# Kernel optimization log

Hardware: AMD Instinct MI355X
Metric: run time of the kernel (lower is better)

## Reference

```python
import jax, jax.numpy as jnp
import numpy as np

DIM = 4096
N_Q_HEADS = 32
N_KV_HEADS = 8
HEAD_DIM = DIM // N_Q_HEADS  # 128
N_REPS = N_Q_HEADS // N_KV_HEADS  # 4
MAX_SEQ = 4096
BATCH = 8
SEQ = 1
START_POS = MAX_SEQ - SEQ  # 4095 (decode step)


def setup_inputs() -> dict:
    key = jax.random.key(0)
    ks = jax.random.split(key, 8)
    s = 0.02
    x = jax.random.normal(ks[0], (BATCH, SEQ, DIM), dtype=jnp.float32)
    wq = jax.random.normal(ks[1], (DIM, N_Q_HEADS * HEAD_DIM), dtype=jnp.float32) * s
    wk = jax.random.normal(ks[2], (DIM, N_KV_HEADS * HEAD_DIM), dtype=jnp.float32) * s
    wv = jax.random.normal(ks[3], (DIM, N_KV_HEADS * HEAD_DIM), dtype=jnp.float32) * s
    wo = jax.random.normal(ks[4], (N_Q_HEADS * HEAD_DIM, DIM), dtype=jnp.float32) * s
    # pre-populated KV cache (decode scenario)
    cache_keys = jax.random.normal(ks[5], (BATCH, MAX_SEQ, N_KV_HEADS, HEAD_DIM), dtype=jnp.float32)
    cache_values = jax.random.normal(ks[6], (BATCH, MAX_SEQ, N_KV_HEADS, HEAD_DIM), dtype=jnp.float32)
    # true RoPE frequencies for positions [START_POS, START_POS+SEQ)
    inv_freq = 1.0 / (10000.0 ** (np.arange(0, HEAD_DIM, 2, dtype=np.float32) / HEAD_DIM))
    pos = np.arange(START_POS, START_POS + SEQ, dtype=np.float32)
    angles = pos[:, None] * inv_freq[None, :]  # [SEQ, HEAD_DIM//2]
    freqs_cos = jnp.asarray(np.cos(angles), dtype=jnp.float32)
    freqs_sin = jnp.asarray(np.sin(angles), dtype=jnp.float32)
    return dict(x=x, start_pos=STAR_POS_INT(), freqs_cos=freqs_cos, freqs_sin=freqs_sin,
                wq=wq, wk=wk, wv=wv, wo=wo,
                cache_keys=cache_keys, cache_values=cache_values)


def STAR_POS_INT():
    return STAR_POS if False else START_POS


def _apply_rope(x, cos, sin):
    # x: [B, S, H, hd]; cos/sin: [S, hd//2]
    xr = x[..., 0::2]
    xi = x[..., 1::2]
    c = cos[None, :, None, :]
    s = sin[None, :, None, :]
    out_r = xr * c - xi * s
    out_i = xr * s + xi * c
    # interleave back: [..., hd//2, 2] -> [..., hd]
    out = jnp.stack([out_r, out_i], axis=-1)
    return out.reshape(x.shape)


def reference(x, start_pos, freqs_cos, freqs_sin, wq, wk, wv, wo, cache_keys, cache_values):
    B, S, _ = x.shape
    q = (x @ wq).reshape(B, S, N_Q_HEADS, HEAD_DIM)
    k = (x @ wk).reshape(B, S, N_KV_HEADS, HEAD_DIM)
    v = (x @ wv).reshape(B, S, N_KV_HEADS, HEAD_DIM)
    q = _apply_rope(q, freqs_cos, freqs_sin)
    k = _apply_rope(k, freqs_cos, freqs_sin)
    # KV-cache scatter write (static start_pos)
    cache_keys = cache_keys.at[:B, start_pos:start_pos + S].set(jax.lax.stop_gradient(k))
    cache_values = cache_values.at[:B, start_pos:start_pos + S].set(jax.lax.stop_gradient(v))
    total = start_pos + S
    keys = cache_keys[:B, :total]     # [B, T, Hkv, hd]
    values = cache_values[:B, :total]
    # repeat_kv: [B, T, Hkv, hd] -> [B, T, Hq, hd]
    keys = jnp.repeat(keys, N_REPS, axis=2)
    values = jnp.repeat(values, N_REPS, axis=2)
    # attention
    scale = 1.0 / jnp.sqrt(jnp.float32(HEAD_DIM))
    scores = jnp.einsum('bshd,bthd->bhst', q, keys) * scale  # [B, Hq, S, T]
    mask = (jnp.arange(total)[None, :] <= (jnp.arange(S)[:, None] + start_pos))  # [S, T]
    scores = jnp.where(mask[None, None], scores, -1e9)
    attn = jax.nn.softmax(scores, axis=-1)
    out = jnp.einsum('bhst,bthd->bshd', attn, values)  # [B, S, Hq, hd]
    out = out.reshape(B, S, N_Q_HEADS * HEAD_DIM)
    return out @ wo
```

## Files before the change

### kernel.cpp

```cpp
#include <hip/hip_runtime.h>

#define DIM 4096
#define HD 128
#define NQH 32
#define NKVH 8
#define NB 8
#define MAXSEQ 4096
#define TOTALT 4096
#define QCOLS (NQH*HD)
#define KVCOLS (NKVH*HD)
#define CCOLS (QCOLS + 2*KVCOLS)
#define DCH 64
#define KSP (DIM/DCH)
#define SUB 32
#define NSUB 16
#define CHK (SUB*NSUB)
#define NCHB (TOTALT/CHK)

typedef __attribute__((address_space(1))) const void __gvoid;
typedef __attribute__((address_space(3))) void __lvoid;
#define GLD16(g, l) __builtin_amdgcn_global_load_lds((__gvoid*)(g), (__lvoid*)(l), 16, 0, 0)
#define VMWAIT(N) asm volatile("s_waitcnt vmcnt(" #N ")" ::: "memory")
#define LGKMWAIT0 asm volatile("s_waitcnt lgkmcnt(0)" ::: "memory")
#define SCHEDBAR __builtin_amdgcn_sched_barrier(0)

__global__ __launch_bounds__(128) void gemv4_kernel(
    const float* __restrict__ x, const float* __restrict__ wq,
    const float* __restrict__ wk, const float* __restrict__ wv,
    float* __restrict__ part, int pstride)
{
    __shared__ float xs[DCH*NB];
    const int tx = threadIdx.x;
    const int d0 = blockIdx.y*DCH;
    for (int i = tx; i < DCH*NB; i += 128)
        xs[(i&63)*NB + (i>>6)] = x[(i>>6)*DIM + d0 + (i&63)];
    __syncthreads();

    const int colbase = blockIdx.x*512;
    const float* w; int wcols, wcol;
    if (colbase < QCOLS)               { w = wq; wcols = QCOLS;  wcol = colbase; }
    else if (colbase < QCOLS+KVCOLS)   { w = wk; wcols = KVCOLS; wcol = colbase - QCOLS; }
    else                               { w = wv; wcols = KVCOLS; wcol = colbase - QCOLS - KVCOLS; }

    const float* wp = w + (size_t)d0*wcols + wcol + tx*4;
    float4 a[NB];
    #pragma unroll
    for (int b = 0; b < NB; b++) { a[b].x=0.f; a[b].y=0.f; a[b].z=0.f; a[b].w=0.f; }

    #pragma unroll 4
    for (int dl = 0; dl < DCH; dl++) {
        float4 wv4 = *reinterpret_cast<const float4*>(wp + (size_t)dl*wcols);
        float4 x0 = *reinterpret_cast<const float4*>(&xs[dl*NB]);
        float4 x1 = *reinterpret_cast<const float4*>(&xs[dl*NB + 4]);
        a[0].x += wv4.x*x0.x; a[0].y += wv4.y*x0.x; a[0].z += wv4.z*x0.x; a[0].w += wv4.w*x0.x;
        a[1].x += wv4.x*x0.y; a[1].y += wv4.y*x0.y; a[1].z += wv4.z*x0.y; a[1].w += wv4.w*x0.y;
        a[2].x += wv4.x*x0.z; a[2].y += wv4.y*x0.z; a[2].z += wv4.z*x0.z; a[2].w += wv4.w*x0.z;
        a[3].x += wv4.x*x0.w; a[3].y += wv4.y*x0.w; a[3].z += wv4.z*x0.w; a[3].w += wv4.w*x0.w;
        a[4].x += wv4.x*x1.x; a[4].y += wv4.y*x1.x; a[4].z += wv4.z*x1.x; a[4].w += wv4.w*x1.x;
        a[5].x += wv4.x*x1.y; a[5].y += wv4.y*x1.y; a[5].z += wv4.z*x1.y; a[5].w += wv4.w*x1.y;
        a[6].x += wv4.x*x1.z; a[6].y += wv4.y*x1.z; a[6].z += wv4.z*x1.z; a[6].w += wv4.w*x1.z;
        a[7].x += wv4.x*x1.w; a[7].y += wv4.y*x1.w; a[7].z += wv4.z*x1.w; a[7].w += wv4.w*x1.w;
    }
    const int ocol = colbase + tx*4;
    #pragma unroll
    for (int b = 0; b < NB; b++)
        *reinterpret_cast<float4*>(&part[((size_t)(blockIdx.y*NB + b))*pstride + ocol]) = a[b];
}

__global__ __launch_bounds__(256) void qkv_reduce_rope(
    const float* __restrict__ part, const float* __restrict__ fc,
    const float* __restrict__ fs, float* __restrict__ q,
    float* __restrict__ knew, float* __restrict__ vnew)
{
    const int p = blockIdx.x*256 + threadIdx.x;
    const int b = p / (CCOLS/2);
    const int c0 = (p % (CCOLS/2))*2;
    float s0 = 0.f, s1 = 0.f;
    const float* pb = part + (size_t)b*CCOLS + c0;
    #pragma unroll 8
    for (int ky = 0; ky < KSP; ky++) {
        float2 v = *reinterpret_cast<const float2*>(pb + (size_t)ky*NB*CCOLS);
        s0 += v.x; s1 += v.y;
    }
    float r0 = s0, r1 = s1;
    if (c0 < QCOLS + KVCOLS) {
        int i = (c0 & (HD-1)) >> 1;
        float c = fc[i], s = fs[i];
        r0 = s0*c - s1*s;
        r1 = s0*s + s1*c;
    }
    if (c0 < QCOLS) {
        *reinterpret_cast<float2*>(&q[b*QCOLS + c0]) = make_float2(r0, r1);
    } else if (c0 < QCOLS + KVCOLS) {
        *reinterpret_cast<float2*>(&knew[b*KVCOLS + (c0 - QCOLS)]) = make_float2(r0, r1);
    } else {
        *reinterpret_cast<float2*>(&vnew[b*KVCOLS + (c0 - QCOLS - KVCOLS)]) = make_float2(r0, r1);
    }
}

__global__ __launch_bounds__(256) void attn_stream_kernel(
    const float* __restrict__ q, const float* __restrict__ knew,
    const float* __restrict__ vnew, const float* __restrict__ K,
    const float* __restrict__ V, float* __restrict__ pout,
    float* __restrict__ pml)
{
    __shared__ float ks[2][SUB*HD];
    __shared__ float vs_[2][SUB*HD];
    __shared__ __align__(16) float psf[SUB*4];
    __shared__ float ps2[16*HD];

    const int tx = threadIdx.x;
    const int chunk = blockIdx.x, kvh = blockIdx.y, b = blockIdx.z;
    const size_t blkid = (size_t)(b*NKVH + kvh)*NCHB + chunk;
    const int lane = tx & 63, j = tx >> 6;
    const int r = lane & 31, h = lane >> 5;
    const size_t kvstride = (size_t)NKVH*HD;
    const size_t kbase0 = ((size_t)(b*MAXSEQ + chunk*CHK)*NKVH + kvh)*HD;
    const bool lastChunk = (chunk == NCHB-1);
    const int wseg = (tx & 192)*4;

    auto stage = [&](int nb, int srow, bool lastT) {
        #pragma unroll
        for (int k = 0; k < 4; k++) {
            int F = k*256 + tx;
            int t = F >> 5, sw = F & 31;
            int i = sw ^ t;
            const float* srck = (lastT && t == SUB-1)
                ? (knew + (b*NKVH + kvh)*HD + i*4)
                : (K + kbase0 + (size_t)(srow + t)*kvstride + i*4);
            GLD16(srck, &ks[nb][k*1024 + wseg]);
            const float* srcv = (lastT && t == SUB-1)
                ? (vnew + (b*NKVH + kvh)*HD + sw*4)
                : (V + kbase0 + (size_t)(srow + t)*kvstride + sw*4);
            GLD16(srcv, &vs_[nb][k*1024 + wseg]);
        }
    };

    float4 qreg[16];
    {
        const float4* qg = reinterpret_cast<const float4*>(
            q + b*QCOLS + (kvh*4 + j)*HD + h*64);
        #pragma unroll
        for (int c = 0; c < 16; c++) qreg[c] = qg[c];
    }
    stage(0, 0, false);

    float2 acc[4];
    #pragma unroll
    for (int hh = 0; hh < 4; hh++) acc[hh] = make_float2(0.f, 0.f);
    float l_lane = 0.f;

    for (int s = 0; s < NSUB; ++s) {
        const int cb = s & 1;
        if (s+1 < NSUB) {
            stage(cb^1, (s+1)*SUB, lastChunk && (s+1 == NSUB-1));
            VMWAIT(8);
        } else {
            VMWAIT(0);
        }
        __builtin_amdgcn_s_barrier();
        SCHEDBAR;

        float sj = 0.f;
        {
            const float* kc = ks[cb];
            #pragma unroll
            for (int c = 0; c < 16; c++) {
                int i = h*16 + c;
                float4 kv = *reinterpret_cast<const float4*>(&kc[(r*32 + (i ^ r))*4]);
                float4 qv = qreg[c];
                sj += kv.x*qv.x + kv.y*qv.y + kv.z*qv.z + kv.w*qv.w;
            }
        }
        sj += __shfl_xor(sj, 32, 64);
        sj *= 0.08838834764831845f;
        float p = __expf(sj);
        l_lane += p;
        if (h == 0) psf[r*4 + j] = p;
        LGKMWAIT0; SCHEDBAR;
        __builtin_amdgcn_s_barrier();
        SCHEDBAR;

        {
            const float* vc = vs_[cb];
            #pragma unroll
            for (int t = 0; t < 8; t++) {
                int row = j*8 + t;
                float4 pg = *reinterpret_cast<const float4*>(&psf[row*4]);
                float2 vv = *reinterpret_cast<const float2*>(&vc[row*HD + lane*2]);
                acc[0].x += pg.x*vv.x; acc[0].y += pg.x*vv.y;
                acc[1].x += pg.y*vv.x; acc[1].y += pg.y*vv.y;
                acc[2].x += pg.z*vv.x; acc[2].y += pg.z*vv.y;
                acc[3].x += pg.w*vv.x; acc[3].y += pg.w*vv.y;
            }
        }
        LGKMWAIT0; SCHEDBAR;
        __builtin_amdgcn_s_barrier();
        SCHEDBAR;
    }

    #pragma unroll
    for (int hh = 0; hh < 4; hh++)
        *reinterpret_cast<float2*>(&ps2[(j*4 + hh)*HD + lane*2]) = acc[hh];
    #pragma unroll
    for (int k = 16; k >= 1; k >>= 1) l_lane += __shfl_xor(l_lane, k, 64);
    if (lane == 0) pml[blkid*4 + j] = l_lane;
    __syncthreads();
    {
        const int hh = tx >> 6;
        const int d0 = (tx & 63)*2;
        float sx = 0.f, sy = 0.f;
        #pragma unroll
        for (int w = 0; w < 4; w++) {
            float2 v = *reinterpret_cast<const float2*>(&ps2[(w*4 + hh)*HD + d0]);
            sx += v.x; sy += v.y;
        }
        *reinterpret_cast<float2*>(pout + blkid*512 + hh*HD + d0) = make_float2(sx, sy);
    }
}

__global__ __launch_bounds__(128) void attn_combine_kernel(
    const float* __restrict__ pout, const float* __restrict__ pml,
    float* __restrict__ attn_out)
{
    const int d = threadIdx.x;
    const int qh = blockIdx.x;
    const int b = blockIdx.y;
    const int kvh = qh >> 2, j = qh & 3;
    const size_t base = (size_t)(b*NKVH + kvh)*NCHB;
    float L = 0.f, acc = 0.f;
    #pragma unroll
    for (int i = 0; i < NCHB; i++) {
        L   += pml[(base + i)*4 + j];
        acc += pout[(base + i)*512 + j*HD + d];
    }
    attn_out[b*QCOLS + qh*HD + d] = acc / L;
}

__global__ __launch_bounds__(256) void wo_reduce_kernel(
    const float* __restrict__ part, float* __restrict__ out)
{
    const int g = blockIdx.x*256 + threadIdx.x;
    float sx = 0.f, sy = 0.f;
    #pragma unroll 8
    for (int ky = 0; ky < KSP; ky++) {
        float2 v = *reinterpret_cast<const float2*>(part + (size_t)ky*NB*QCOLS + g*2);
        sx += v.x; sy += v.y;
    }
    *reinterpret_cast<float2*>(out + g*2) = make_float2(sx, sy);
}

extern "C" void kernel_launch(void* const* d_in, const int* in_sizes, int n_in,
                              void* d_out, int out_size, void* d_ws, size_t ws_size,
                              hipStream_t stream)
{
    const float* x  = (const float*)d_in[0];
    const float* fc = (const float*)d_in[2];
    const float* fs = (const float*)d_in[3];
    const float* wq = (const float*)d_in[4];
    const float* wk = (const float*)d_in[5];
    const float* wv = (const float*)d_in[6];
    const float* wo = (const float*)d_in[7];
    const float* K  = (const float*)d_in[8];
    const float* V  = (const float*)d_in[9];

    float* ws     = (float*)d_ws;
    float* q      = ws;
    float* knew   = ws + 32768;
    float* vnew   = ws + 40960;
    float* attn_o = ws + 49152;
    float* qkvp   = ws + 81920;
    float* pout   = ws + 3227648;
    float* pml    = ws + 3489792;
    float* wop    = ws + 81920;

    gemv4_kernel<<<dim3(CCOLS/512, KSP), dim3(128), 0, stream>>>(x, wq, wk, wv, qkvp, CCOLS);
    qkv_reduce_rope<<<dim3(NB*CCOLS/2/256), dim3(256), 0, stream>>>(qkvp, fc, fs, q, knew, vnew);
    attn_stream_kernel<<<dim3(NCHB, NKVH, NB), dim3(256), 0, stream>>>(q, knew, vnew, K, V, pout, pml);
    attn_combine_kernel<<<dim3(NQH, NB), dim3(128), 0, stream>>>(pout, pml, attn_o);
    gemv4_kernel<<<dim3(QCOLS/512, KSP), dim3(128), 0, stream>>>(attn_o, wo, wo, wo, wop, QCOLS);
    wo_reduce_kernel<<<dim3(NB*QCOLS/2/256), dim3(256), 0, stream>>>(wop, (float*)d_out);
}
```

Baseline: 119.9 us.

## Process all KV heads per block over contiguous full cache rows

The attention streaming kernel now gives each block a 128-timestep chunk covering all 8 KV heads, staging full contiguous 4KB cache rows, 8 rows per tile, instead of strided per-head 512B segments. It uses 512 threads, one wave per KV head, with an XOR swizzle to avoid LDS bank conflicts. The goal is more sequential DRAM access for the dominant KV-cache read. In exchange the grid halves to 256 blocks and each block takes about 128KB of double-buffered LDS, which limits a CU to one resident block. The per-chunk partial outputs also grow, so the combine kernel has more data to write and read.

```diff
diff --git a/kernel.cpp b/kernel.cpp
--- a/kernel.cpp
+++ b/kernel.cpp
@@ -12,10 +12,10 @@
 #define CCOLS (QCOLS + 2*KVCOLS)
 #define DCH 64
 #define KSP (DIM/DCH)
-#define SUB 32
-#define NSUB 16
-#define CHK (SUB*NSUB)
-#define NCHB (TOTALT/CHK)
+#define RT 8
+#define NT 16
+#define CHKR (RT*NT)
+#define NCHK (TOTALT/CHKR)
 
 typedef __attribute__((address_space(1))) const void __gvoid;
 typedef __attribute__((address_space(3))) void __lvoid;
@@ -98,62 +98,64 @@
     }
 }
 
-__global__ __launch_bounds__(256) void attn_stream_kernel(
+__global__ __launch_bounds__(512) void attn_fullrow_kernel(
     const float* __restrict__ q, const float* __restrict__ knew,
     const float* __restrict__ vnew, const float* __restrict__ K,
     const float* __restrict__ V, float* __restrict__ pout,
     float* __restrict__ pml)
 {
-    __shared__ float ks[2][SUB*HD];
-    __shared__ float vs_[2][SUB*HD];
-    __shared__ __align__(16) float psf[SUB*4];
-    __shared__ float ps2[16*HD];
+    __shared__ float ks[2][RT*KVCOLS];
+    __shared__ float vs[2][RT*KVCOLS];
+    __shared__ __align__(16) float psf[NKVH*RT*4];
 
     const int tx = threadIdx.x;
-    const int chunk = blockIdx.x, kvh = blockIdx.y, b = blockIdx.z;
-    const size_t blkid = (size_t)(b*NKVH + kvh)*NCHB + chunk;
-    const int lane = tx & 63, j = tx >> 6;
-    const int r = lane & 31, h = lane >> 5;
-    const size_t kvstride = (size_t)NKVH*HD;
-    const size_t kbase0 = ((size_t)(b*MAXSEQ + chunk*CHK)*NKVH + kvh)*HD;
-    const bool lastChunk = (chunk == NCHB-1);
-    const int wseg = (tx & 192)*4;
+    const int chunk = blockIdx.x, b = blockIdx.y;
+    const int w = tx >> 6, lane = tx & 63;
+    const int r = lane >> 3, seg = lane & 7;
+    const size_t blkid = (size_t)b*NCHK + chunk;
+    const size_t base0 = ((size_t)b*MAXSEQ + (size_t)chunk*CHKR)*KVCOLS;
+    const bool lastChunk = (chunk == NCHK-1);
 
     auto stage = [&](int nb, int srow, bool lastT) {
         #pragma unroll
         for (int k = 0; k < 4; k++) {
-            int F = k*256 + tx;
-            int t = F >> 5, sw = F & 31;
-            int i = sw ^ t;
-            const float* srck = (lastT && t == SUB-1)
-                ? (knew + (b*NKVH + kvh)*HD + i*4)
-                : (K + kbase0 + (size_t)(srow + t)*kvstride + i*4);
-            GLD16(srck, &ks[nb][k*1024 + wseg]);
-            const float* srcv = (lastT && t == SUB-1)
-                ? (vnew + (b*NKVH + kvh)*HD + sw*4)
-                : (V + kbase0 + (size_t)(srow + t)*kvstride + sw*4);
-            GLD16(srcv, &vs_[nb][k*1024 + wseg]);
+            const int Lbase = k*512 + w*64;
+            const int rr = Lbase >> 8;
+            const int L = Lbase + lane;
+            const int g = L & 255;
+            const int gk = (g & ~7) | ((g & 7) ^ rr);
+            const float* srck = (lastT && rr == RT-1)
+                ? (knew + b*KVCOLS + gk*4)
+                : (K + base0 + (size_t)(srow + rr)*KVCOLS + gk*4);
+            GLD16(srck, &ks[nb][(size_t)Lbase*4]);
+            const float* srcv = (lastT && rr == RT-1)
+                ? (vnew + b*KVCOLS + g*4)
+                : (V + base0 + (size_t)(srow + rr)*KVCOLS + g*4);
+            GLD16(srcv, &vs[nb][(size_t)Lbase*4]);
         }
     };
 
     float4 qreg[16];
     {
-        const float4* qg = reinterpret_cast<const float4*>(
-            q + b*QCOLS + (kvh*4 + j)*HD + h*64);
-        #pragma unroll
-        for (int c = 0; c < 16; c++) qreg[c] = qg[c];
+        #pragma unroll
+        for (int hh = 0; hh < 4; hh++) {
+            const float4* qg = reinterpret_cast<const float4*>(
+                q + b*QCOLS + (w*4 + hh)*HD + seg*16);
+            #pragma unroll
+            for (int c = 0; c < 4; c++) qreg[hh*4 + c] = qg[c];
+        }
     }
     stage(0, 0, false);
 
     float2 acc[4];
     #pragma unroll
     for (int hh = 0; hh < 4; hh++) acc[hh] = make_float2(0.f, 0.f);
-    float l_lane = 0.f;
-
-    for (int s = 0; s < NSUB; ++s) {
+    float l_acc[4] = {0.f, 0.f, 0.f, 0.f};
+
+    for (int s = 0; s < NT; ++s) {
         const int cb = s & 1;
-        if (s+1 < NSUB) {
-            stage(cb^1, (s+1)*SUB, lastChunk && (s+1 == NSUB-1));
+        if (s+1 < NT) {
+            stage(cb^1, (s+1)*RT, lastChunk && (s+1 == NT-1));
             VMWAIT(8);
         } else {
             VMWAIT(0);
@@ -161,33 +163,44 @@
         __builtin_amdgcn_s_barrier();
         SCHEDBAR;
 
-        float sj = 0.f;
+        float s4[4] = {0.f, 0.f, 0.f, 0.f};
         {
             const float* kc = ks[cb];
             #pragma unroll
-            for (int c = 0; c < 16; c++) {
-                int i = h*16 + c;
-                float4 kv = *reinterpret_cast<const float4*>(&kc[(r*32 + (i ^ r))*4]);
-                float4 qv = qreg[c];
-                sj += kv.x*qv.x + kv.y*qv.y + kv.z*qv.z + kv.w*qv.w;
+            for (int c = 0; c < 4; c++) {
+                int g  = w*32 + seg*4 + c;
+                int gs = (g & ~7) | ((g & 7) ^ r);
+                float4 kv = *reinterpret_cast<const float4*>(&kc[(r*256 + gs)*4]);
+                #pragma unroll
+                for (int hh = 0; hh < 4; hh++) {
+                    float4 qv = qreg[hh*4 + c];
+                    s4[hh] += kv.x*qv.x + kv.y*qv.y + kv.z*qv.z + kv.w*qv.w;
+                }
             }
         }
-        sj += __shfl_xor(sj, 32, 64);
-        sj *= 0.08838834764831845f;
-        float p = __expf(sj);
-        l_lane += p;
-        if (h == 0) psf[r*4 + j] = p;
+        #pragma unroll
+        for (int m = 1; m <= 4; m <<= 1) {
+            #pragma unroll
+            for (int hh = 0; hh < 4; hh++) s4[hh] += __shfl_xor(s4[hh], m, 64);
+        }
+        float p0 = __expf(s4[0]*0.08838834764831845f);
+        float p1 = __expf(s4[1]*0.08838834764831845f);
+        float p2 = __expf(s4[2]*0.08838834764831845f);
+        float p3 = __expf(s4[3]*0.08838834764831845f);
+        l_acc[0] += p0; l_acc[1] += p1; l_acc[2] += p2; l_acc[3] += p3;
+        if (seg == 0)
+            *reinterpret_cast<float4*>(&psf[(w*RT + r)*4]) = make_float4(p0, p1, p2, p3);
         LGKMWAIT0; SCHEDBAR;
         __builtin_amdgcn_s_barrier();
         SCHEDBAR;
 
         {
-            const float* vc = vs_[cb];
-            #pragma unroll
-            for (int t = 0; t < 8; t++) {
-                int row = j*8 + t;
-                float4 pg = *reinterpret_cast<const float4*>(&psf[row*4]);
-                float2 vv = *reinterpret_cast<const float2*>(&vc[row*HD + lane*2]);
+            const float* vc = vs[cb];
+            #pragma unroll
+            for (int t = 0; t < RT; t++) {
+                float4 pg = *reinterpret_cast<const float4*>(&psf[(w*RT + t)*4]);
+                float2 vv = *reinterpret_cast<const float2*>(
+                    &vc[t*KVCOLS + w*HD + lane*2]);
                 acc[0].x += pg.x*vv.x; acc[0].y += pg.x*vv.y;
                 acc[1].x += pg.y*vv.x; acc[1].y += pg.y*vv.y;
                 acc[2].x += pg.z*vv.x; acc[2].y += pg.z*vv.y;
@@ -201,21 +214,17 @@
 
     #pragma unroll
     for (int hh = 0; hh < 4; hh++)
-        *reinterpret_cast<float2*>(&ps2[(j*4 + hh)*HD + lane*2]) = acc[hh];
-    #pragma unroll
-    for (int k = 16; k >= 1; k >>= 1) l_lane += __shfl_xor(l_lane, k, 64);
-    if (lane == 0) pml[blkid*4 + j] = l_lane;
-    __syncthreads();
-    {
-        const int hh = tx >> 6;
-        const int d0 = (tx & 63)*2;
-        float sx = 0.f, sy = 0.f;
-        #pragma unroll
-        for (int w = 0; w < 4; w++) {
-            float2 v = *reinterpret_cast<const float2*>(&ps2[(w*4 + hh)*HD + d0]);
-            sx += v.x; sy += v.y;
-        }
-        *reinterpret_cast<float2*>(pout + blkid*512 + hh*HD + d0) = make_float2(sx, sy);
+        *reinterpret_cast<float2*>(
+            pout + blkid*4096 + (w*4 + hh)*HD + lane*2) = acc[hh];
+    #pragma unroll
+    for (int m = 1; m <= 32; m <<= 1) {
+        #pragma unroll
+        for (int hh = 0; hh < 4; hh++) l_acc[hh] += __shfl_xor(l_acc[hh], m, 64);
+    }
+    if (lane == 0) {
+        #pragma unroll
+        for (int hh = 0; hh < 4; hh++)
+            pml[blkid*NQH + w*4 + hh] = l_acc[hh]*0.125f;
     }
 }
 
@@ -226,13 +235,12 @@
     const int d = threadIdx.x;
     const int qh = blockIdx.x;
     const int b = blockIdx.y;
-    const int kvh = qh >> 2, j = qh & 3;
-    const size_t base = (size_t)(b*NKVH + kvh)*NCHB;
     float L = 0.f, acc = 0.f;
-    #pragma unroll
-    for (int i = 0; i < NCHB; i++) {
-        L   += pml[(base + i)*4 + j];
-        acc += pout[(base + i)*512 + j*HD + d];
+    #pragma unroll 8
+    for (int i = 0; i < NCHK; i++) {
+        const size_t blkid = (size_t)b*NCHK + i;
+        L   += pml[blkid*NQH + qh];
+        acc += pout[blkid*4096 + qh*HD + d];
     }
     attn_out[b*QCOLS + qh*HD + d] = acc / L;
 }
@@ -271,12 +279,12 @@
     float* attn_o = ws + 49152;
     float* qkvp   = ws + 81920;
     float* pout   = ws + 3227648;
-    float* pml    = ws + 3489792;
+    float* pml    = ws + 4276224;
     float* wop    = ws + 81920;
 
     gemv4_kernel<<<dim3(CCOLS/512, KSP), dim3(128), 0, stream>>>(x, wq, wk, wv, qkvp, CCOLS);
     qkv_reduce_rope<<<dim3(NB*CCOLS/2/256), dim3(256), 0, stream>>>(qkvp, fc, fs, q, knew, vnew);
-    attn_stream_kernel<<<dim3(NCHB, NKVH, NB), dim3(256), 0, stream>>>(q, knew, vnew, K, V, pout, pml);
+    attn_fullrow_kernel<<<dim3(NCHK, NB), dim3(512), 0, stream>>>(q, knew, vnew, K, V, pout, pml);
     attn_combine_kernel<<<dim3(NQH, NB), dim3(128), 0, stream>>>(pout, pml, attn_o);
     gemv4_kernel<<<dim3(QCOLS/512, KSP), dim3(128), 0, stream>>>(attn_o, wo, wo, wo, wop, QCOLS);
     wo_reduce_kernel<<<dim3(NB*QCOLS/2/256), dim3(256), 0, stream>>>(wop, (float*)d_out);
```

New measurement: 128.7 us. 7.3% more time.

## Stream V directly from global memory and shrink attention chunks for more blocks

Applied to the files above, without the earlier changes.

The attention kernel now stages only K through LDS. V rows are read straight from global memory into registers and weighted by the probabilities shared in LDS. The chunk size drops from 512 to 128 tokens, which quadruples the grid and raises occupancy via launch bounds. This removes the V LDS traffic, one barrier per tile and the final LDS reduction, in exchange for a larger partial-output buffer and more work in the combine kernel. The vmcnt wait counts are retuned for the K-only staging.

```diff
diff --git a/kernel.cpp b/kernel.cpp
--- a/kernel.cpp
+++ b/kernel.cpp
@@ -13,9 +13,9 @@
 #define DCH 64
 #define KSP (DIM/DCH)
 #define SUB 32
-#define NSUB 16
-#define CHK (SUB*NSUB)
-#define NCHB (TOTALT/CHK)
+#define NTL 4
+#define CHKR (SUB*NTL)
+#define NCHB (TOTALT/CHKR)
 
 typedef __attribute__((address_space(1))) const void __gvoid;
 typedef __attribute__((address_space(3))) void __lvoid;
@@ -98,26 +98,24 @@
     }
 }
 
-__global__ __launch_bounds__(256) void attn_stream_kernel(
+__global__ __launch_bounds__(256, 4) void attn_v6_kernel(
     const float* __restrict__ q, const float* __restrict__ knew,
     const float* __restrict__ vnew, const float* __restrict__ K,
     const float* __restrict__ V, float* __restrict__ pout,
     float* __restrict__ pml)
 {
     __shared__ float ks[2][SUB*HD];
-    __shared__ float vs_[2][SUB*HD];
-    __shared__ __align__(16) float psf[SUB*4];
-    __shared__ float ps2[16*HD];
+    __shared__ __align__(16) float psf[4][SUB];
 
     const int tx = threadIdx.x;
     const int chunk = blockIdx.x, kvh = blockIdx.y, b = blockIdx.z;
     const size_t blkid = (size_t)(b*NKVH + kvh)*NCHB + chunk;
     const int lane = tx & 63, j = tx >> 6;
     const int r = lane & 31, h = lane >> 5;
+    const int rp = lane >> 5, dq = lane & 31;
     const size_t kvstride = (size_t)NKVH*HD;
-    const size_t kbase0 = ((size_t)(b*MAXSEQ + chunk*CHK)*NKVH + kvh)*HD;
+    const size_t kbase0 = ((size_t)(b*MAXSEQ + chunk*CHKR)*NKVH + kvh)*HD;
     const bool lastChunk = (chunk == NCHB-1);
-    const int wseg = (tx & 192)*4;
 
     auto stage = [&](int nb, int srow, bool lastT) {
         #pragma unroll
@@ -128,11 +126,7 @@
             const float* srck = (lastT && t == SUB-1)
                 ? (knew + (b*NKVH + kvh)*HD + i*4)
                 : (K + kbase0 + (size_t)(srow + t)*kvstride + i*4);
-            GLD16(srck, &ks[nb][k*1024 + wseg]);
-            const float* srcv = (lastT && t == SUB-1)
-                ? (vnew + (b*NKVH + kvh)*HD + sw*4)
-                : (V + kbase0 + (size_t)(srow + t)*kvstride + sw*4);
-            GLD16(srcv, &vs_[nb][k*1024 + wseg]);
+            GLD16(srck, &ks[nb][((tx & 192)*4) + k*1024]);
         }
     };
 
@@ -145,18 +139,16 @@
     }
     stage(0, 0, false);
 
-    float2 acc[4];
-    #pragma unroll
-    for (int hh = 0; hh < 4; hh++) acc[hh] = make_float2(0.f, 0.f);
+    float4 acc = make_float4(0.f, 0.f, 0.f, 0.f);
     float l_lane = 0.f;
 
-    for (int s = 0; s < NSUB; ++s) {
+    for (int s = 0; s < NTL; ++s) {
         const int cb = s & 1;
-        if (s+1 < NSUB) {
-            stage(cb^1, (s+1)*SUB, lastChunk && (s+1 == NSUB-1));
-            VMWAIT(8);
+        if (s+1 < NTL) {
+            stage(cb^1, (s+1)*SUB, lastChunk && (s+1 == NTL-1));
+            if (s == 0) { VMWAIT(4); } else { VMWAIT(20); }
         } else {
-            VMWAIT(0);
+            VMWAIT(16);
         }
         __builtin_amdgcn_s_barrier();
         SCHEDBAR;
@@ -176,47 +168,49 @@
         sj *= 0.08838834764831845f;
         float p = __expf(sj);
         l_lane += p;
-        if (h == 0) psf[r*4 + j] = p;
+        if (h == 0) psf[j][r] = p;
         LGKMWAIT0; SCHEDBAR;
         __builtin_amdgcn_s_barrier();
         SCHEDBAR;
 
         {
-            const float* vc = vs_[cb];
-            #pragma unroll
-            for (int t = 0; t < 8; t++) {
-                int row = j*8 + t;
-                float4 pg = *reinterpret_cast<const float4*>(&psf[row*4]);
-                float2 vv = *reinterpret_cast<const float2*>(&vc[row*HD + lane*2]);
-                acc[0].x += pg.x*vv.x; acc[0].y += pg.x*vv.y;
-                acc[1].x += pg.y*vv.x; acc[1].y += pg.y*vv.y;
-                acc[2].x += pg.z*vv.x; acc[2].y += pg.z*vv.y;
-                acc[3].x += pg.w*vv.x; acc[3].y += pg.w*vv.y;
+            const float* vbase = V + kbase0
+                + (size_t)(s*SUB + rp)*kvstride + dq*4;
+            if (!(lastChunk && s == NTL-1)) {
+                #pragma unroll
+                for (int t = 0; t < 16; t++) {
+                    float4 vv = *reinterpret_cast<const float4*>(
+                        vbase + (size_t)(2*t)*kvstride);
+                    float2 pp = *reinterpret_cast<const float2*>(&psf[j][2*t]);
+                    float pw = rp ? pp.y : pp.x;
+                    acc.x += pw*vv.x; acc.y += pw*vv.y;
+                    acc.z += pw*vv.z; acc.w += pw*vv.w;
+                }
+            } else {
+                #pragma unroll
+                for (int t = 0; t < 16; t++) {
+                    const float* vp = (t == 15 && rp == 1)
+                        ? (vnew + (b*NKVH + kvh)*HD + dq*4)
+                        : (vbase + (size_t)(2*t)*kvstride);
+                    float4 vv = *reinterpret_cast<const float4*>(vp);
+                    float2 pp = *reinterpret_cast<const float2*>(&psf[j][2*t]);
+                    float pw = rp ? pp.y : pp.x;
+                    acc.x += pw*vv.x; acc.y += pw*vv.y;
+                    acc.z += pw*vv.z; acc.w += pw*vv.w;
+                }
             }
         }
-        LGKMWAIT0; SCHEDBAR;
-        __builtin_amdgcn_s_barrier();
-        SCHEDBAR;
-    }
-
-    #pragma unroll
-    for (int hh = 0; hh < 4; hh++)
-        *reinterpret_cast<float2*>(&ps2[(j*4 + hh)*HD + lane*2]) = acc[hh];
+    }
+
+    acc.x += __shfl_xor(acc.x, 32, 64);
+    acc.y += __shfl_xor(acc.y, 32, 64);
+    acc.z += __shfl_xor(acc.z, 32, 64);
+    acc.w += __shfl_xor(acc.w, 32, 64);
     #pragma unroll
     for (int k = 16; k >= 1; k >>= 1) l_lane += __shfl_xor(l_lane, k, 64);
+    if (rp == 0)
+        *reinterpret_cast<float4*>(pout + blkid*512 + j*HD + dq*4) = acc;
     if (lane == 0) pml[blkid*4 + j] = l_lane;
-    __syncthreads();
-    {
-        const int hh = tx >> 6;
-        const int d0 = (tx & 63)*2;
-        float sx = 0.f, sy = 0.f;
-        #pragma unroll
-        for (int w = 0; w < 4; w++) {
-            float2 v = *reinterpret_cast<const float2*>(&ps2[(w*4 + hh)*HD + d0]);
-            sx += v.x; sy += v.y;
-        }
-        *reinterpret_cast<float2*>(pout + blkid*512 + hh*HD + d0) = make_float2(sx, sy);
-    }
 }
 
 __global__ __launch_bounds__(128) void attn_combine_kernel(
@@ -229,7 +223,7 @@
     const int kvh = qh >> 2, j = qh & 3;
     const size_t base = (size_t)(b*NKVH + kvh)*NCHB;
     float L = 0.f, acc = 0.f;
-    #pragma unroll
+    #pragma unroll 8
     for (int i = 0; i < NCHB; i++) {
         L   += pml[(base + i)*4 + j];
         acc += pout[(base + i)*512 + j*HD + d];
@@ -271,12 +265,12 @@
     float* attn_o = ws + 49152;
     float* qkvp   = ws + 81920;
     float* pout   = ws + 3227648;
-    float* pml    = ws + 3489792;
+    float* pml    = ws + 4276224;
     float* wop    = ws + 81920;
 
     gemv4_kernel<<<dim3(CCOLS/512, KSP), dim3(128), 0, stream>>>(x, wq, wk, wv, qkvp, CCOLS);
     qkv_reduce_rope<<<dim3(NB*CCOLS/2/256), dim3(256), 0, stream>>>(qkvp, fc, fs, q, knew, vnew);
-    attn_stream_kernel<<<dim3(NCHB, NKVH, NB), dim3(256), 0, stream>>>(q, knew, vnew, K, V, pout, pml);
+    attn_v6_kernel<<<dim3(NCHB, NKVH, NB), dim3(256), 0, stream>>>(q, knew, vnew, K, V, pout, pml);
     attn_combine_kernel<<<dim3(NQH, NB), dim3(128), 0, stream>>>(pout, pml, attn_o);
     gemv4_kernel<<<dim3(QCOLS/512, KSP), dim3(128), 0, stream>>>(attn_o, wo, wo, wo, wop, QCOLS);
     wo_reduce_kernel<<<dim3(NB*QCOLS/2/256), dim3(256), 0, stream>>>(wop, (float*)d_out);
```

New measurement: 225.0 us. 1.88x slower.
